# Kernel optimization log

Hardware: AMD Instinct MI355X
Metric: run time of the kernel (lower is better)

## Reference

```python
import jax, jax.numpy as jnp
import numpy as np

H = 32        # num heads
D = 80        # head dim
HID = 2560    # hidden size = H*D
ROT = 32      # rotary dim = int(0.4*80)
THETA = 10000.0
T = 2048      # total packed tokens
B = 4         # sequences
SEQ = 512     # tokens per sequence
CACHE = 4096  # paged cache slots


def setup_inputs() -> dict:
    key = jax.random.key(0)
    ks = jax.random.split(key, 10)
    bound = 1.0 / np.sqrt(HID)

    def lin(k):
        kw, kb = jax.random.split(k)
        W = jax.random.uniform(kw, (HID, HID), jnp.float32, -bound, bound)
        b = jax.random.uniform(kb, (HID,), jnp.float32, -bound, bound)
        return W, b

    Wq, bq = lin(ks[0])
    Wk, bk = lin(ks[1])
    Wv, bv = lin(ks[2])
    Wd, bd = lin(ks[3])
    h = jax.random.normal(ks[4], (T, HID), jnp.float32)
    return {
        "h": h,
        "k_cache": jnp.zeros((CACHE, HID), jnp.float32),
        "v_cache": jnp.zeros((CACHE, HID), jnp.float32),
        "positions": (jnp.arange(T) % SEQ).astype(jnp.int32),
        "offsets": (jnp.arange(B + 1) * SEQ).astype(jnp.int32),
        "cache_indices": jnp.arange(T, dtype=jnp.int32),
        "Wq": Wq, "bq": bq, "Wk": Wk, "bk": bk,
        "Wv": Wv, "bv": bv, "Wd": Wd, "bd": bd,
    }


def _rotate_half(x):
    x1, x2 = jnp.split(x, 2, axis=-1)
    return jnp.concatenate([-x2, x1], axis=-1)


def reference(h, k_cache, v_cache, positions, offsets, cache_indices,
              Wq, bq, Wk, bk, Wv, bv, Wd, bd):
    # QKV projections (torch Linear: x @ W.T + b)
    q = h @ Wq.T + bq
    k = h @ Wk.T + bk
    v = h @ Wv.T + bv

    q3 = q.reshape(T, H, D)
    k3 = k.reshape(T, H, D)

    # partial RoPE on first ROT dims of each head
    pos = positions.astype(jnp.float32)
    inv_freq = 1.0 / (THETA ** (jnp.arange(0, ROT, 2, dtype=jnp.float32) / ROT))
    freqs = pos[:, None] * inv_freq                      # [T, ROT/2]
    emb = jnp.concatenate([freqs, freqs], axis=-1)       # [T, ROT]
    cos = jnp.cos(emb)[:, None, :]                       # [T, 1, ROT]
    sin = jnp.sin(emb)[:, None, :]

    q_rot, q_pass = q3[..., :ROT], q3[..., ROT:]
    k_rot, k_pass = k3[..., :ROT], k3[..., ROT:]
    q_rot = q_rot * cos + _rotate_half(q_rot) * sin
    k_rot = k_rot * cos + _rotate_half(k_rot) * sin
    q3 = jnp.concatenate([q_rot, q_pass], axis=-1)
    k3 = jnp.concatenate([k_rot, k_pass], axis=-1)

    # prompt_init=True path: scatter rotated k and v into paged caches
    new_k_cache = k_cache.at[cache_indices].set(k3.reshape(T, HID))
    new_v_cache = v_cache.at[cache_indices].set(v)

    # variable-length causal attention over packed sequences
    scale = D ** -0.5
    scores = jnp.einsum('thd,shd->hts', q3, k3) * scale   # [H, T, T]
    idx = jnp.arange(T)
    seg = jnp.searchsorted(offsets[1:], idx, side='right')
    mask = (seg[:, None] == seg[None, :]) & (idx[:, None] >= idx[None, :])
    scores = jnp.where(mask[None], scores, jnp.float32(-1e30))
    p = jax.nn.softmax(scores, axis=-1)
    o = jnp.einsum('hts,shd->thd', p, v.reshape(T, H, D)).reshape(T, HID)

    out = o @ Wd.T + bd
    return out, new_k_cache, new_v_cache
```

## Files before the change

### kernel.cpp

```cpp
#include <hip/hip_runtime.h>
#include <cstdint>
#include <cstddef>


#define HIDDEN 2560
#define SEQT 2048
#define NHEADS 32
#define DHEAD 80
#define NSEG 4
#define SEGLEN 512
#define CACHE_ROWS 4096
#define QSCALE 0.11180339887498949f

typedef __bf16 bf16_8 __attribute__((ext_vector_type(8)));
typedef unsigned short u16x8 __attribute__((ext_vector_type(8)));
typedef float f32x4 __attribute__((ext_vector_type(4)));

__device__ __forceinline__ unsigned short f2bf(float f) {
  unsigned int u = __builtin_bit_cast(unsigned int, f);
  u += 0x7fffu + ((u >> 16) & 1u);
  return (unsigned short)(u >> 16);
}
__device__ __forceinline__ float bf2f(unsigned short s) {
  unsigned int u = ((unsigned int)s) << 16;
  return __builtin_bit_cast(float, u);
}

__device__ __forceinline__ void gload16(const unsigned short* g, unsigned short* l) {
  __builtin_amdgcn_global_load_lds(
      (const __attribute__((address_space(1))) unsigned int*)g,
      (__attribute__((address_space(3))) unsigned int*)l, 16, 0, 0);
}

#define BAR() asm volatile("s_barrier" ::: "memory")
#define LGKM0()                                          \
  do {                                                   \
    asm volatile("s_waitcnt lgkmcnt(0)" ::: "memory");   \
    __builtin_amdgcn_sched_barrier(0);                   \
  } while (0)
#define PRIO(x) __builtin_amdgcn_s_setprio(x)
#define MF(af, bf, c) c = __builtin_amdgcn_mfma_f32_16x16x32_bf16(af, bf, c, 0, 0, 0)

__global__ __launch_bounds__(256) void cast_kernel(
    const float* __restrict__ src, unsigned short* __restrict__ dst, int n4) {
  int i = blockIdx.x * blockDim.x + threadIdx.x;
  const int stride = gridDim.x * blockDim.x;
  for (; i < n4; i += stride) {
    float4 v = ((const float4*)src)[i];
    ushort4 o;
    o.x = f2bf(v.x); o.y = f2bf(v.y); o.z = f2bf(v.z); o.w = f2bf(v.w);
    ((ushort4*)dst)[i] = o;
  }
}

__global__ __launch_bounds__(256) void cast4_kernel(
    const float* __restrict__ s0, const float* __restrict__ s1,
    const float* __restrict__ s2, const float* __restrict__ s3,
    unsigned short* __restrict__ d0, unsigned short* __restrict__ d1,
    unsigned short* __restrict__ d2, unsigned short* __restrict__ d3, int n4) {
  const float* s = blockIdx.z == 0 ? s0 : blockIdx.z == 1 ? s1 : blockIdx.z == 2 ? s2 : s3;
  unsigned short* d = blockIdx.z == 0 ? d0 : blockIdx.z == 1 ? d1 : blockIdx.z == 2 ? d2 : d3;
  int i = blockIdx.x * blockDim.x + threadIdx.x;
  const int stride = gridDim.x * blockDim.x;
  for (; i < n4; i += stride) {
    float4 v = ((const float4*)s)[i];
    ushort4 o;
    o.x = f2bf(v.x); o.y = f2bf(v.y); o.z = f2bf(v.z); o.w = f2bf(v.w);
    ((ushort4*)d)[i] = o;
  }
}

template <bool BF16OUT>
__device__ __forceinline__ void gemm256_body(
    const unsigned short* __restrict__ A, const unsigned short* __restrict__ Bg,
    const float* __restrict__ bias, void* __restrict__ C) {
  constexpr int K = HIDDEN;
  constexpr int NT = K / 64;
  __shared__ __align__(16) unsigned short L[65536];

  const int tid = threadIdx.x;
  const int lane = tid & 63;
  const int wid = tid >> 6;
  const int l15 = lane & 15;
  const int kg = lane >> 4;
  const int wm = wid >> 2;
  const int wn = wid & 3;
  const int m0 = blockIdx.x * 256;
  const int n0 = blockIdx.y * 256;

  const int g8 = (((tid & 7) - (tid >> 3)) & 7) * 8;
  const int srow = tid >> 3;
  const unsigned short* As0 = A + (size_t)(m0 + srow) * K + g8;
  const unsigned short* As1 = As0 + (size_t)128 * K;
  const unsigned short* Bs0 = Bg + (size_t)(n0 + srow) * K + g8;
  const unsigned short* Bs1 = Bs0 + (size_t)128 * K;
  const int t16 = tid * 8;

  auto stA0 = [&](int kt) {
    const int b = (kt & 1) * 32768, ko = kt * 64;
    gload16(As0 + ko, L + b + t16);
    gload16(As1 + ko, L + b + 8192 + t16);
  };
  auto stA1 = [&](int kt) {
    const int b = (kt & 1) * 32768, ko = 64 * K + kt * 64;
    gload16(As0 + ko, L + b + 4096 + t16);
    gload16(As1 + ko, L + b + 12288 + t16);
  };
  auto stB0 = [&](int kt) {
    const int b = (kt & 1) * 32768 + 16384, ko = kt * 64;
    gload16(Bs0 + ko, L + b + t16);
    gload16(Bs0 + 64 * K + ko, L + b + 4096 + t16);
  };
  auto stB1 = [&](int kt) {
    const int b = (kt & 1) * 32768 + 16384 + 8192, ko = kt * 64;
    gload16(Bs1 + ko, L + b + t16);
    gload16(Bs1 + 64 * K + ko, L + b + 4096 + t16);
  };

  const int c0 = (kg + l15) & 7;
  const int aof0 = wm * 8192 + l15 * 64 + c0 * 8;
  const int aof1 = wm * 8192 + l15 * 64 + (c0 ^ 4) * 8;
  const int bof0 = 16384 + wn * 4096 + l15 * 64 + c0 * 8;
  const int bof1 = 16384 + wn * 4096 + l15 * 64 + (c0 ^ 4) * 8;

  f32x4 acc[8][4];
#pragma unroll
  for (int m = 0; m < 8; m++)
#pragma unroll
    for (int n = 0; n < 4; n++) acc[m][n] = f32x4{0.f, 0.f, 0.f, 0.f};

  bf16_8 a[4][2], bl[2][2], bh[2][2];

#define DSR(off) (*(const bf16_8*)(L + (off)))
  auto rdA = [&](int off) {
#pragma unroll
    for (int fm = 0; fm < 4; fm++) {
      a[fm][0] = DSR(off + aof0 + fm * 1024);
      a[fm][1] = DSR(off + aof1 + fm * 1024);
    }
  };
  auto rdBl = [&](int off) {
#pragma unroll
    for (int fn = 0; fn < 2; fn++) {
      bl[fn][0] = DSR(off + bof0 + fn * 1024);
      bl[fn][1] = DSR(off + bof1 + fn * 1024);
    }
  };
  auto rdBh = [&](int off) {
#pragma unroll
    for (int fn = 0; fn < 2; fn++) {
      bh[fn][0] = DSR(off + bof0 + (2 + fn) * 1024);
      bh[fn][1] = DSR(off + bof1 + (2 + fn) * 1024);
    }
  };
  auto mmq = [&](int mq, int nq, bf16_8 (&bb)[2][2]) {
#pragma unroll
    for (int fm = 0; fm < 4; fm++)
#pragma unroll
      for (int fn = 0; fn < 2; fn++) {
        MF(a[fm][0], bb[fn][0], acc[mq * 4 + fm][nq * 2 + fn]);
        MF(a[fm][1], bb[fn][1], acc[mq * 4 + fm][nq * 2 + fn]);
      }
  };

  stA0(0); stB0(0); stB1(0); stA1(0);
  stA0(1); stB0(1); stB1(1);
  asm volatile("s_waitcnt vmcnt(6)" ::: "memory");
  BAR();

#pragma unroll 2
  for (int t = 0; t < NT - 2; ++t) {
    const int bo = (t & 1) * 32768;
    rdA(bo); rdBl(bo);
    stA1(t + 1);
    BAR(); LGKM0(); PRIO(1); mmq(0, 0, bl); PRIO(0); BAR();
    rdBh(bo);
    stA0(t + 2);
    BAR(); LGKM0(); PRIO(1); mmq(0, 1, bh); PRIO(0); BAR();
    rdA(bo + 4096);
    stB0(t + 2);
    BAR(); LGKM0(); PRIO(1); mmq(1, 0, bl); PRIO(0); BAR();
    stB1(t + 2);
    BAR(); PRIO(1); mmq(1, 1, bh); PRIO(0);
    asm volatile("s_waitcnt vmcnt(6)" ::: "memory");
    BAR();
  }

  {
    const int bo = 0;
    rdA(bo); rdBl(bo);
    stA1(39);
    BAR(); LGKM0(); PRIO(1); mmq(0, 0, bl); PRIO(0); BAR();
    rdBh(bo);
    BAR(); LGKM0(); PRIO(1); mmq(0, 1, bh); PRIO(0); BAR();
    rdA(bo + 4096);
    BAR(); LGKM0(); PRIO(1); mmq(1, 0, bl); PRIO(0); BAR();
    BAR(); PRIO(1); mmq(1, 1, bh); PRIO(0);
    asm volatile("s_waitcnt vmcnt(0)" ::: "memory");
    BAR();
  }
  {
    const int bo = 32768;
    rdA(bo); rdBl(bo);
    BAR(); LGKM0(); PRIO(1); mmq(0, 0, bl); PRIO(0); BAR();
    rdBh(bo);
    BAR(); LGKM0(); PRIO(1); mmq(0, 1, bh); PRIO(0); BAR();
    rdA(bo + 4096);
    BAR(); LGKM0(); PRIO(1); mmq(1, 0, bl); PRIO(0); BAR();
    PRIO(1); mmq(1, 1, bh); PRIO(0);
  }
#undef DSR

#pragma unroll
  for (int n4 = 0; n4 < 4; n4++) {
    const int col = n0 + wn * 64 + n4 * 16 + l15;
    const float bv = bias[col];
#pragma unroll
    for (int m8 = 0; m8 < 8; m8++) {
      const int rowb = m0 + wm * 128 + m8 * 16 + kg * 4;
#pragma unroll
      for (int j = 0; j < 4; j++) {
        float val = acc[m8][n4][j] + bv;
        if (BF16OUT)
          ((unsigned short*)C)[(size_t)(rowb + j) * HIDDEN + col] = f2bf(val);
        else
          ((float*)C)[(size_t)(rowb + j) * HIDDEN + col] = val;
      }
    }
  }
}

__global__ __launch_bounds__(512, 2) void gemm_qkv8_kernel(
    const unsigned short* __restrict__ A,
    const unsigned short* __restrict__ B0, const unsigned short* __restrict__ B1,
    const unsigned short* __restrict__ B2,
    const float* __restrict__ bias0, const float* __restrict__ bias1,
    const float* __restrict__ bias2,
    unsigned short* __restrict__ C0, unsigned short* __restrict__ C1,
    unsigned short* __restrict__ C2) {
  const unsigned short* B = blockIdx.z == 0 ? B0 : (blockIdx.z == 1 ? B1 : B2);
  const float* bias = blockIdx.z == 0 ? bias0 : (blockIdx.z == 1 ? bias1 : bias2);
  unsigned short* C = blockIdx.z == 0 ? C0 : (blockIdx.z == 1 ? C1 : C2);
  gemm256_body<true>(A, B, bias, C);
}

__global__ __launch_bounds__(512, 2) void gemm_out8_kernel(
    const unsigned short* __restrict__ A, const unsigned short* __restrict__ B,
    const float* __restrict__ bias, float* __restrict__ C) {
  gemm256_body<false>(A, B, bias, C);
}

__global__ __launch_bounds__(256) void rope_scatter_kernel(
    unsigned short* __restrict__ qb, unsigned short* __restrict__ kb,
    const unsigned short* __restrict__ vb,
    const int* __restrict__ positions, const int* __restrict__ cidx,
    float* __restrict__ kco, float* __restrict__ vco) {
  const int t = blockIdx.x;
  const int tid = threadIdx.x;
  __shared__ float cs[16], sn[16];

  if (tid < 16) {
    const float pos = (float)positions[t];
    const float inv = expf(-(float)tid * (9.210340371976184f / 16.0f));
    const float f = pos * inv;
    cs[tid] = cosf(f);
    sn[tid] = sinf(f);
  }
  __syncthreads();

  for (int i = tid; i < 1024; i += 256) {
    const int which = i >> 9;
    const int p = i & 511;
    const int hh = p >> 4, d = p & 15;
    unsigned short* buf = which ? kb : qb;
    const size_t base = (size_t)t * HIDDEN + hh * DHEAD + d;
    const float x1 = bf2f(buf[base]);
    const float x2 = bf2f(buf[base + 16]);
    const float c = cs[d], s = sn[d];
    buf[base] = f2bf(x1 * c - x2 * s);
    buf[base + 16] = f2bf(x2 * c + x1 * s);
  }
  __syncthreads();

  const int ci = cidx[t];
  float* krow = kco + (size_t)ci * HIDDEN;
  float* vrow = vco + (size_t)ci * HIDDEN;
  const unsigned short* ks = kb + (size_t)t * HIDDEN;
  const unsigned short* vs = vb + (size_t)t * HIDDEN;
  for (int i = tid; i < HIDDEN; i += 256) {
    krow[i] = bf2f(ks[i]);
    vrow[i] = bf2f(vs[i]);
  }
}

#define KSTR 104
#define VSTR 72
#define PSTR 72

__global__ __launch_bounds__(256) void attn_mfma_kernel(
    const unsigned short* __restrict__ qb, const unsigned short* __restrict__ kb,
    const unsigned short* __restrict__ vb, unsigned short* __restrict__ ob) {
  const int qt = blockIdx.x;
  const int h = blockIdx.y;
  const int seg = blockIdx.z;
  const int tq0 = seg * SEGLEN + qt * 64;

  __shared__ unsigned short Kt[64 * KSTR];
  __shared__ unsigned short VtT[80 * VSTR];
  __shared__ unsigned short Pw[4][16 * PSTR];

  const int tid = threadIdx.x;
  const int lane = tid & 63;
  const int w = tid >> 6;
  const int l15 = lane & 15;
  const int g = lane >> 4;

  bf16_8 qa[3];
  {
    const unsigned short* qp = qb + (size_t)(tq0 + w * 16 + l15) * HIDDEN + h * DHEAD;
#pragma unroll
    for (int c = 0; c < 3; c++) {
      u16x8 t = (u16x8)(unsigned short)0;
      const int d0 = c * 32 + g * 8;
      if (d0 < DHEAD) {
#pragma unroll
        for (int e = 0; e < 8; e++) t[e] = f2bf(bf2f(qp[d0 + e]) * QSCALE);
      }
      qa[c] = __builtin_bit_cast(bf16_8, t);
    }
  }

  float m_[4], l_[4];
#pragma unroll
  for (int j = 0; j < 4; j++) { m_[j] = -3.0e38f; l_[j] = 0.f; }
  f32x4 Oacc[5];
#pragma unroll
  for (int n = 0; n < 5; n++) Oacc[n] = f32x4{0.f, 0.f, 0.f, 0.f};

  for (int st = 0; st <= qt; ++st) {
    const int ts0 = seg * SEGLEN + st * 64;
    __syncthreads();
    for (int i = tid; i < 64 * 20; i += 256) {
      const int row = i / 20;
      const int c = i - row * 20;
      const size_t gsrc = (size_t)(ts0 + row) * HIDDEN + h * DHEAD + c * 4;
      ushort4 kv = *(const ushort4*)(kb + gsrc);
      ushort4 vv = *(const ushort4*)(vb + gsrc);
      *(ushort4*)&Kt[row * KSTR + c * 4] = kv;
      VtT[(c * 4 + 0) * VSTR + row] = vv.x;
      VtT[(c * 4 + 1) * VSTR + row] = vv.y;
      VtT[(c * 4 + 2) * VSTR + row] = vv.z;
      VtT[(c * 4 + 3) * VSTR + row] = vv.w;
    }
    __syncthreads();

    f32x4 Sacc[4];
#pragma unroll
    for (int t = 0; t < 4; t++) Sacc[t] = f32x4{0.f, 0.f, 0.f, 0.f};
#pragma unroll
    for (int c = 0; c < 3; c++) {
#pragma unroll
      for (int t = 0; t < 4; t++) {
        bf16_8 kf;
        if (c < 2 || g < 2)
          kf = *(const bf16_8*)&Kt[(t * 16 + l15) * KSTR + c * 32 + g * 8];
        else
          kf = __builtin_bit_cast(bf16_8, (u16x8)(unsigned short)0);
        Sacc[t] = __builtin_amdgcn_mfma_f32_16x16x32_bf16(qa[c], kf, Sacc[t], 0, 0, 0);
      }
    }

    if (st == qt) {
#pragma unroll
      for (int t = 0; t < 4; t++)
#pragma unroll
        for (int j = 0; j < 4; j++)
          if (t * 16 + l15 > w * 16 + 4 * g + j) Sacc[t][j] = -1e30f;
    }

    float pm[4], ps[4], rold[4];
#pragma unroll
    for (int j = 0; j < 4; j++)
      pm[j] = fmaxf(fmaxf(Sacc[0][j], Sacc[1][j]), fmaxf(Sacc[2][j], Sacc[3][j]));
#pragma unroll
    for (int d = 1; d < 16; d <<= 1)
#pragma unroll
      for (int j = 0; j < 4; j++) pm[j] = fmaxf(pm[j], __shfl_xor(pm[j], d, 64));
#pragma unroll
    for (int j = 0; j < 4; j++) {
      const float mn = fmaxf(m_[j], pm[j]);
      rold[j] = __expf(m_[j] - mn);
      m_[j] = mn;
      ps[j] = 0.f;
    }
#pragma unroll
    for (int t = 0; t < 4; t++)
#pragma unroll
      for (int j = 0; j < 4; j++) {
        const float p = __expf(Sacc[t][j] - m_[j]);
        Sacc[t][j] = p;
        ps[j] += p;
      }
#pragma unroll
    for (int d = 1; d < 16; d <<= 1)
#pragma unroll
      for (int j = 0; j < 4; j++) ps[j] += __shfl_xor(ps[j], d, 64);
#pragma unroll
    for (int j = 0; j < 4; j++) l_[j] = l_[j] * rold[j] + ps[j];

#pragma unroll
    for (int t = 0; t < 4; t++)
#pragma unroll
      for (int j = 0; j < 4; j++)
        Pw[w][(4 * g + j) * PSTR + t * 16 + l15] = f2bf(Sacc[t][j]);
#pragma unroll
    for (int n = 0; n < 5; n++)
#pragma unroll
      for (int j = 0; j < 4; j++) Oacc[n][j] *= rold[j];

#pragma unroll
    for (int c = 0; c < 2; c++) {
      bf16_8 pa = *(const bf16_8*)&Pw[w][l15 * PSTR + c * 32 + g * 8];
#pragma unroll
      for (int n = 0; n < 5; n++) {
        bf16_8 vf = *(const bf16_8*)&VtT[(n * 16 + l15) * VSTR + c * 32 + g * 8];
        Oacc[n] = __builtin_amdgcn_mfma_f32_16x16x32_bf16(pa, vf, Oacc[n], 0, 0, 0);
      }
    }
  }

  float inv[4];
#pragma unroll
  for (int j = 0; j < 4; j++) inv[j] = 1.f / l_[j];
  unsigned short* op = ob + (size_t)(tq0 + w * 16) * HIDDEN + h * DHEAD;
#pragma unroll
  for (int n = 0; n < 5; n++)
#pragma unroll
    for (int j = 0; j < 4; j++)
      op[(size_t)(4 * g + j) * HIDDEN + n * 16 + l15] = f2bf(Oacc[n][j] * inv[j]);
}

extern "C" void kernel_launch(void* const* d_in, const int* in_sizes, int n_in,
                              void* d_out, int out_size, void* d_ws, size_t ws_size,
                              hipStream_t stream) {
  const float* h = (const float*)d_in[0];
  const float* kci = (const float*)d_in[1];
  const float* vci = (const float*)d_in[2];
  const int* positions = (const int*)d_in[3];
  const int* cidx = (const int*)d_in[5];
  const float* Wq = (const float*)d_in[6];
  const float* bq = (const float*)d_in[7];
  const float* Wk = (const float*)d_in[8];
  const float* bk = (const float*)d_in[9];
  const float* Wv = (const float*)d_in[10];
  const float* bv = (const float*)d_in[11];
  const float* Wd = (const float*)d_in[12];
  const float* bd = (const float*)d_in[13];

  float* out = (float*)d_out;
  float* kco = out + (size_t)SEQT * HIDDEN;
  float* vco = kco + (size_t)CACHE_ROWS * HIDDEN;

  char* ws = (char*)d_ws;
  unsigned short* h_bf = (unsigned short*)ws;  ws += (size_t)SEQT * HIDDEN * 2;
  unsigned short* Wq_bf = (unsigned short*)ws; ws += (size_t)HIDDEN * HIDDEN * 2;
  unsigned short* Wk_bf = (unsigned short*)ws; ws += (size_t)HIDDEN * HIDDEN * 2;
  unsigned short* Wv_bf = (unsigned short*)ws; ws += (size_t)HIDDEN * HIDDEN * 2;
  unsigned short* Wd_bf = (unsigned short*)ws; ws += (size_t)HIDDEN * HIDDEN * 2;
  unsigned short* q_bf = (unsigned short*)ws;  ws += (size_t)SEQT * HIDDEN * 2;
  unsigned short* k_bf = (unsigned short*)ws;  ws += (size_t)SEQT * HIDDEN * 2;
  unsigned short* v_bf = (unsigned short*)ws;  ws += (size_t)SEQT * HIDDEN * 2;
  unsigned short* o_bf = (unsigned short*)ws;  ws += (size_t)SEQT * HIDDEN * 2;

  const size_t half = (size_t)SEQT * HIDDEN;
  hipMemcpyAsync(kco + half, kci + half, half * 4, hipMemcpyDeviceToDevice, stream);
  hipMemcpyAsync(vco + half, vci + half, half * 4, hipMemcpyDeviceToDevice, stream);

  cast_kernel<<<2048, 256, 0, stream>>>(h, h_bf, SEQT * HIDDEN / 4);
  {
    dim3 gc(2048, 1, 4);
    cast4_kernel<<<gc, 256, 0, stream>>>(Wq, Wk, Wv, Wd, Wq_bf, Wk_bf, Wv_bf, Wd_bf,
                                         HIDDEN * HIDDEN / 4);
  }

  {
    dim3 gq(SEQT / 256, HIDDEN / 256, 3);
    gemm_qkv8_kernel<<<gq, 512, 0, stream>>>(h_bf, Wq_bf, Wk_bf, Wv_bf, bq, bk, bv,
                                             q_bf, k_bf, v_bf);
  }

  rope_scatter_kernel<<<SEQT, 256, 0, stream>>>(q_bf, k_bf, v_bf, positions, cidx, kco, vco);

  {
    dim3 ga(SEGLEN / 64, NHEADS, NSEG);
    attn_mfma_kernel<<<ga, 256, 0, stream>>>(q_bf, k_bf, v_bf, o_bf);
  }

  {
    dim3 go(SEQT / 256, HIDDEN / 256, 1);
    gemm_out8_kernel<<<go, 512, 0, stream>>>(o_bf, Wd_bf, bd, out);
  }
}
```

Before: 275.1 us.

## Split-K the output projection GEMM and swizzle GEMM block order

The output projection GEMM is split into two K halves, which doubles its block count from 80 to 160 so more of the GPU's compute units have work. Each half writes fp32 partial sums into workspace buffers that reuse the space of dead bf16 inputs and weights. A new reduce kernel then adds the two partials and the bias. Both GEMMs also remap linear block IDs with a swizzle so that blocks running together share more A and B tiles in cache. The cost is an extra launch plus roughly 63MB of additional fp32 traffic for the partials.

```diff
diff --git a/kernel.cpp b/kernel.cpp
--- a/kernel.cpp
+++ b/kernel.cpp
@@ -70,12 +70,13 @@
   }
 }
 
-template <bool BF16OUT>
+template <int OUTMODE, int NT>
 __device__ __forceinline__ void gemm256_body(
     const unsigned short* __restrict__ A, const unsigned short* __restrict__ Bg,
-    const float* __restrict__ bias, void* __restrict__ C) {
+    const float* __restrict__ bias, void* __restrict__ C,
+    int m0, int n0, int kbase) {
   constexpr int K = HIDDEN;
-  constexpr int NT = K / 64;
+  static_assert((NT & 1) == 0 && NT >= 4, "NT must be even");
   __shared__ __align__(16) unsigned short L[65536];
 
   const int tid = threadIdx.x;
@@ -85,14 +86,12 @@
   const int kg = lane >> 4;
   const int wm = wid >> 2;
   const int wn = wid & 3;
-  const int m0 = blockIdx.x * 256;
-  const int n0 = blockIdx.y * 256;
 
   const int g8 = (((tid & 7) - (tid >> 3)) & 7) * 8;
   const int srow = tid >> 3;
-  const unsigned short* As0 = A + (size_t)(m0 + srow) * K + g8;
+  const unsigned short* As0 = A + (size_t)(m0 + srow) * K + kbase + g8;
   const unsigned short* As1 = As0 + (size_t)128 * K;
-  const unsigned short* Bs0 = Bg + (size_t)(n0 + srow) * K + g8;
+  const unsigned short* Bs0 = Bg + (size_t)(n0 + srow) * K + kbase + g8;
   const unsigned short* Bs1 = Bs0 + (size_t)128 * K;
   const int t16 = tid * 8;
 
@@ -189,7 +188,7 @@
   {
     const int bo = 0;
     rdA(bo); rdBl(bo);
-    stA1(39);
+    stA1(NT - 1);
     BAR(); LGKM0(); PRIO(1); mmq(0, 0, bl); PRIO(0); BAR();
     rdBh(bo);
     BAR(); LGKM0(); PRIO(1); mmq(0, 1, bh); PRIO(0); BAR();
@@ -214,14 +213,14 @@
 #pragma unroll
   for (int n4 = 0; n4 < 4; n4++) {
     const int col = n0 + wn * 64 + n4 * 16 + l15;
-    const float bv = bias[col];
+    const float bv = (OUTMODE == 2) ? 0.f : bias[col];
 #pragma unroll
     for (int m8 = 0; m8 < 8; m8++) {
       const int rowb = m0 + wm * 128 + m8 * 16 + kg * 4;
 #pragma unroll
       for (int j = 0; j < 4; j++) {
         float val = acc[m8][n4][j] + bv;
-        if (BF16OUT)
+        if (OUTMODE == 0)
           ((unsigned short*)C)[(size_t)(rowb + j) * HIDDEN + col] = f2bf(val);
         else
           ((float*)C)[(size_t)(rowb + j) * HIDDEN + col] = val;
@@ -238,16 +237,48 @@
     const float* __restrict__ bias2,
     unsigned short* __restrict__ C0, unsigned short* __restrict__ C1,
     unsigned short* __restrict__ C2) {
-  const unsigned short* B = blockIdx.z == 0 ? B0 : (blockIdx.z == 1 ? B1 : B2);
-  const float* bias = blockIdx.z == 0 ? bias0 : (blockIdx.z == 1 ? bias1 : bias2);
-  unsigned short* C = blockIdx.z == 0 ? C0 : (blockIdx.z == 1 ? C1 : C2);
-  gemm256_body<true>(A, B, bias, C);
+  const int lb = blockIdx.x + 8 * (blockIdx.y + 10 * blockIdx.z);
+  const int swz = (lb & 7) * 30 + (lb >> 3);
+  const int mx = swz & 7;
+  const int r = swz >> 3;
+  const int ny = r % 10;
+  const int zz = r / 10;
+  const unsigned short* B = zz == 0 ? B0 : (zz == 1 ? B1 : B2);
+  const float* bias = zz == 0 ? bias0 : (zz == 1 ? bias1 : bias2);
+  unsigned short* C = zz == 0 ? C0 : (zz == 1 ? C1 : C2);
+  gemm256_body<0, 40>(A, B, bias, C, mx * 256, ny * 256, 0);
 }
 
 __global__ __launch_bounds__(512, 2) void gemm_out8_kernel(
     const unsigned short* __restrict__ A, const unsigned short* __restrict__ B,
-    const float* __restrict__ bias, float* __restrict__ C) {
-  gemm256_body<false>(A, B, bias, C);
+    float* __restrict__ P0, float* __restrict__ P1) {
+  const int lb = blockIdx.x + 8 * (blockIdx.y + 10 * blockIdx.z);
+  const int swz = (lb & 7) * 20 + (lb >> 3);
+  const int mx = swz & 7;
+  const int r = swz >> 3;
+  const int ny = r % 10;
+  const int kz = r / 10;
+  float* P = kz == 0 ? P0 : P1;
+  gemm256_body<2, 20>(A, B, nullptr, P, mx * 256, ny * 256, kz * 1280);
+}
+
+__global__ __launch_bounds__(256) void reduce_bias_kernel(
+    const float* __restrict__ p0, const float* __restrict__ p1,
+    const float* __restrict__ bias, float* __restrict__ out, int n4) {
+  int i = blockIdx.x * blockDim.x + threadIdx.x;
+  const int stride = gridDim.x * blockDim.x;
+  for (; i < n4; i += stride) {
+    float4 a = ((const float4*)p0)[i];
+    float4 b = ((const float4*)p1)[i];
+    const int cb = (i * 4) % HIDDEN;
+    float4 bv = *(const float4*)&bias[cb];
+    float4 o;
+    o.x = a.x + b.x + bv.x;
+    o.y = a.y + b.y + bv.y;
+    o.z = a.z + b.z + bv.z;
+    o.w = a.w + b.w + bv.w;
+    ((float4*)out)[i] = o;
+  }
 }
 
 __global__ __launch_bounds__(256) void rope_scatter_kernel(
@@ -462,6 +493,7 @@
   float* vco = kco + (size_t)CACHE_ROWS * HIDDEN;
 
   char* ws = (char*)d_ws;
+  char* ws0 = ws;
   unsigned short* h_bf = (unsigned short*)ws;  ws += (size_t)SEQT * HIDDEN * 2;
   unsigned short* Wq_bf = (unsigned short*)ws; ws += (size_t)HIDDEN * HIDDEN * 2;
   unsigned short* Wk_bf = (unsigned short*)ws; ws += (size_t)HIDDEN * HIDDEN * 2;
@@ -472,6 +504,9 @@
   unsigned short* v_bf = (unsigned short*)ws;  ws += (size_t)SEQT * HIDDEN * 2;
   unsigned short* o_bf = (unsigned short*)ws;  ws += (size_t)SEQT * HIDDEN * 2;
 
+  float* part0 = (float*)ws0;
+  float* part1 = part0 + (size_t)SEQT * HIDDEN;
+
   const size_t half = (size_t)SEQT * HIDDEN;
   hipMemcpyAsync(kco + half, kci + half, half * 4, hipMemcpyDeviceToDevice, stream);
   hipMemcpyAsync(vco + half, vci + half, half * 4, hipMemcpyDeviceToDevice, stream);
@@ -497,7 +532,9 @@
   }
 
   {
-    dim3 go(SEQT / 256, HIDDEN / 256, 1);
-    gemm_out8_kernel<<<go, 512, 0, stream>>>(o_bf, Wd_bf, bd, out);
-  }
-}
+    dim3 go(SEQT / 256, HIDDEN / 256, 2);
+    gemm_out8_kernel<<<go, 512, 0, stream>>>(o_bf, Wd_bf, part0, part1);
+  }
+  reduce_bias_kernel<<<2048, 256, 0, stream>>>(part0, part1, bd, out,
+                                               SEQT * HIDDEN / 4);
+}
```

New measurement: 259.4 us. 1.06x faster.
